# Kernel tuning notes

Hardware: AMD Instinct MI355X
Metric: run time of the kernel (lower is better)

The kernel has to match this reference:

```python
import jax, jax.numpy as jnp
import numpy as np

N = 512      # num_nodes
B = 32       # batch
T = 12       # encoder seq_len
HOR = 12     # decoder horizon
U = 64       # rnn_units
K = 2        # max_diffusion_step
M = 2 * K + 1  # num_matrices (2 supports)


def setup_inputs() -> dict:
    key = jax.random.key(0)
    ks = jax.random.split(key, 16)

    # dual random-walk supports: (D^-1 A)^T and (D^-1 A^T)^T, with self loops
    adj = (jax.random.uniform(ks[0], (N, N)) < 32.0 / N).astype(jnp.float32)

    def rw_T(a):
        a = a + jnp.eye(N, dtype=jnp.float32)
        return (a / a.sum(axis=1, keepdims=True)).T

    supports = jnp.stack([rw_T(adj), rw_T(adj.T)])  # (2, N, N)

    def w(k, shape, s=0.1):
        return jax.random.normal(k, shape, dtype=jnp.float32) * s

    Cin0 = (1 + U) * M   # layer0: input_dim(1)+units, times num_matrices
    Cin1 = (U + U) * M   # layer1
    return {
        "inputs": jax.random.normal(ks[1], (T, B, N * 1), dtype=jnp.float32),
        "supports": supports,
        "enc0_Wg": w(ks[2], (Cin0, 2 * U)), "enc0_bg": jnp.ones(2 * U, jnp.float32),
        "enc0_Wc": w(ks[3], (Cin0, U)),     "enc0_bc": jnp.zeros(U, jnp.float32),
        "enc1_Wg": w(ks[4], (Cin1, 2 * U)), "enc1_bg": jnp.ones(2 * U, jnp.float32),
        "enc1_Wc": w(ks[5], (Cin1, U)),     "enc1_bc": jnp.zeros(U, jnp.float32),
        "dec0_Wg": w(ks[6], (Cin0, 2 * U)), "dec0_bg": jnp.ones(2 * U, jnp.float32),
        "dec0_Wc": w(ks[7], (Cin0, U)),     "dec0_bc": jnp.zeros(U, jnp.float32),
        "dec1_Wg": w(ks[8], (Cin1, 2 * U)), "dec1_bg": jnp.ones(2 * U, jnp.float32),
        "dec1_Wc": w(ks[9], (Cin1, U)),     "dec1_bc": jnp.zeros(U, jnp.float32),
        "proj_W": w(ks[10], (U, 1)),        "proj_b": jnp.zeros(1, jnp.float32),
    }


def reference(inputs, supports, enc0_Wg, enc0_bg, enc0_Wc, enc0_bc,
              enc1_Wg, enc1_bg, enc1_Wc, enc1_bc,
              dec0_Wg, dec0_bg, dec0_Wc, dec0_bc,
              dec1_Wg, dec1_bg, dec1_Wc, dec1_bc, proj_W, proj_b):
    Bsz = inputs.shape[1]

    def gconv(x0, W, b):
        # x0: (B, N, C); Chebyshev-style diffusion over each support
        xs = [x0]
        for i in range(supports.shape[0]):
            s = supports[i]
            x1 = jnp.einsum('ij,bjc->bic', s, x0)
            xs.append(x1)
            xp, xpp = x1, x0
            for _ in range(K - 1):
                x2 = 2.0 * jnp.einsum('ij,bjc->bic', s, xp) - xpp
                xs.append(x2)
                xp, xpp = x2, xp
        # stack on last axis to match torch's (B,N,C,num_matrices) -> (B*N, C*M) layout
        z = jnp.stack(xs, axis=-1).reshape(Bsz, N, -1)
        return z @ W + b

    def cell(x, h, Wg, bg, Wc, bc):
        g = jax.nn.sigmoid(gconv(jnp.concatenate([x, h], axis=-1), Wg, bg))
        r, u = jnp.split(g, 2, axis=-1)
        c = jnp.tanh(gconv(jnp.concatenate([x, r * h], axis=-1), Wc, bc))
        return u * h + (1.0 - u) * c

    h0 = jnp.zeros((Bsz, N, U), inputs.dtype)
    h1 = jnp.zeros((Bsz, N, U), inputs.dtype)

    def enc_step(carry, xt):
        h0, h1 = carry
        x = xt.reshape(Bsz, N, 1)
        h0 = cell(x, h0, enc0_Wg, enc0_bg, enc0_Wc, enc0_bc)
        h1 = cell(h0, h1, enc1_Wg, enc1_bg, enc1_Wc, enc1_bc)
        return (h0, h1), None

    (h0, h1), _ = jax.lax.scan(enc_step, (h0, h1), inputs)

    def dec_step(carry, _):
        h0, h1, xin = carry
        h0 = cell(xin, h0, dec0_Wg, dec0_bg, dec0_Wc, dec0_bc)
        h1 = cell(h0, h1, dec1_Wg, dec1_bg, dec1_Wc, dec1_bc)
        out = h1 @ proj_W + proj_b        # (B, N, 1)
        return (h0, h1, out), out.reshape(Bsz, N)

    go = jnp.zeros((Bsz, N, 1), inputs.dtype)
    _, outs = jax.lax.scan(dec_step, (h0, h1, go), None, length=HOR)
    return outs  # (horizon, B, N*output_dim)
```

## Files before the change

kernel.cpp:

```cpp
#include <hip/hip_runtime.h>
#include <math.h>

#define NN 512
#define BB 32
#define TT 12
#define HH 12
#define UU 64
#define CAP 128
#define RTOT (NN * BB)

__device__ __forceinline__ float sigm(float x) { return 1.f / (1.f + expf(-x)); }

__global__ __launch_bounds__(256) void build_ell(const float* __restrict__ sup,
                                                 int2* __restrict__ ell8,
                                                 int2* __restrict__ ell4,
                                                 int* __restrict__ ecnt) {
    int wave = (blockIdx.x * blockDim.x + threadIdx.x) >> 6;
    int lane = threadIdx.x & 63;
    if (wave >= 2 * NN) return;
    const float* row = sup + (size_t)wave * NN;
    int base = 0;
    for (int k = 0; k < NN / 64; ++k) {
        float v = row[k * 64 + lane];
        unsigned long long m = __ballot(v != 0.0f);
        int pre = __popcll(m & ((1ull << lane) - 1ull));
        if (v != 0.0f) {
            int pos = base + pre;
            if (pos < CAP) {
                int j = k * 64 + lane;
                int vb = __float_as_int(v);
                ell8[(size_t)pos * 1024 + wave] = make_int2(j * 32 + ((j >> 2) & 1) * 16, vb);
                ell4[(size_t)pos * 1024 + wave] = make_int2(j * 16, vb);
            }
        }
        base += __popcll(m);
    }
    if (lane == 0) ecnt[wave] = base < CAP ? base : CAP;
}

__global__ void zero_kernel(float* __restrict__ p, int n) {
    int i = blockIdx.x * 256 + threadIdx.x;
    if (i < n) p[i] = 0.0f;
}

__global__ void wmax_kernel(const int* __restrict__ ecnt, int* __restrict__ wmax) {
    int g = threadIdx.x;
    if (g >= 16) return;
    int s = g >> 3, grp = g & 7;
    int m = 0;
    for (int i = 0; i < 64; ++i) {
        int c = ecnt[s * NN + grp * 64 + i];
        m = c > m ? c : m;
    }
    wmax[g] = m;
}

__global__ void wprep(const float* __restrict__ src, float* __restrict__ dstP,
                      float* __restrict__ dstX, int C, int OO, int WD, int L0) {
    int idx = blockIdx.x * 256 + threadIdx.x;
    int total = 5 * C * OO;
    if (idx >= total) return;
    int oi = idx % WD;
    int rem = idx / WD;
    int c = rem % C;
    int rem2 = rem / C;
    int m = rem2 % 5;
    int oq = rem2 / 5;
    int o = oq * WD + oi;
    int crow = L0 ? (c + 1) : c;
    size_t base = (size_t)crow * 5 * OO + o;
    float v;
    if (m == 0) v = src[base] - src[base + 2 * OO] - src[base + 4 * OO];
    else        v = src[base + (size_t)m * OO];
    dstP[idx] = v;
    if (L0 && c == 0) {
        size_t b0 = (size_t)o;
        float xvv;
        if (m == 0) xvv = src[b0] - src[b0 + 2 * OO] - src[b0 + 4 * OO];
        else        xvv = src[b0 + (size_t)m * OO];
        dstX[(oq * 5 + m) * WD + oi] = xvv;
    }
}

template<bool L0, bool GATE>
__global__ __launch_bounds__(512) void fused(const float* __restrict__ hA,
                                             const float* __restrict__ hB,
                                             const float* __restrict__ g,
                                             const float* __restrict__ Wp,
                                             const float* __restrict__ Xr,
                                             const float* __restrict__ xv,
                                             const float* __restrict__ bias,
                                             const int2* __restrict__ ell,
                                             const int* __restrict__ wmax,
                                             float* __restrict__ gout,
                                             const float* __restrict__ hOld,
                                             float* __restrict__ hNew) {
    constexpr int C  = L0 ? 64 : 128;
    constexpr int WD = GATE ? 8 : 4;

    __shared__ float S[512 * WD * 2];
    float* T0 = S;
    float* T1 = S + 512 * WD;

    int bid = blockIdx.x;
    int swz = (bid & 7) * 64 + (bid >> 3);
    int b = swz >> 4, oq = swz & 15;
    int o0 = oq * WD;
    int n = threadIdx.x;
    int wm0 = wmax[n >> 6];
    int wm1 = wmax[8 + (n >> 6)];
    float xn = L0 ? xv[b * 512 + n] : 0.f;

    const float* Wb = Wp + (size_t)oq * 5 * C * WD;
    float acc[5][WD];
    #pragma unroll
    for (int oi = 0; oi < WD; ++oi) acc[0][oi] = bias[o0 + oi];
    #pragma unroll
    for (int m = 1; m < 5; ++m)
        #pragma unroll
        for (int oi = 0; oi < WD; ++oi) acc[m][oi] = 0.f;

    #pragma unroll 2
    for (int c = 0; c < C; ++c) {
        float a;
        if (L0) {
            if (GATE) a = hA[(size_t)((b << 6) + c) * 512 + n];
            else      a = g[(size_t)((b << 7) + c) * 512 + n];
        } else {
            if (c < 64) {
                a = hA[(size_t)((b << 6) + c) * 512 + n];
            } else {
                int u = c - 64;
                if (GATE) a = hB[(size_t)((b << 6) + u) * 512 + n];
                else      a = g[(size_t)((b << 7) + u) * 512 + n];
            }
        }
        #pragma unroll
        for (int m = 0; m < 5; ++m) {
            const float* wrow = Wb + ((size_t)m * C + c) * WD;
            #pragma unroll
            for (int oi = 0; oi < WD; ++oi)
                acc[m][oi] += a * wrow[oi];
        }
    }

    if (L0) {
        const float* xr = Xr + (size_t)oq * 5 * WD;
        #pragma unroll
        for (int m = 0; m < 5; ++m)
            #pragma unroll
            for (int oi = 0; oi < WD; ++oi)
                acc[m][oi] += xn * xr[m * WD + oi];
    }

    float uval[WD], hval[WD];
    if (!GATE) {
        #pragma unroll
        for (int oi = 0; oi < WD; ++oi) {
            uval[oi] = g[(size_t)((b << 7) + 64 + o0 + oi) * 512 + n];
            hval[oi] = hOld[(size_t)((b << 6) + o0 + oi) * 512 + n];
        }
    }

    int hsel = (n >> 2) & 1;
    if constexpr (WD == 8) {
        *(float4*)&T0[n * 8 + hsel * 4] =
            make_float4(acc[2][0], acc[2][1], acc[2][2], acc[2][3]);
        *(float4*)&T0[n * 8 + (hsel ^ 1) * 4] =
            make_float4(acc[2][4], acc[2][5], acc[2][6], acc[2][7]);
        *(float4*)&T1[n * 8 + hsel * 4] =
            make_float4(acc[4][0], acc[4][1], acc[4][2], acc[4][3]);
        *(float4*)&T1[n * 8 + (hsel ^ 1) * 4] =
            make_float4(acc[4][4], acc[4][5], acc[4][6], acc[4][7]);
    } else {
        *(float4*)&T0[n * 4] = make_float4(acc[2][0], acc[2][1], acc[2][2], acc[2][3]);
        *(float4*)&T1[n * 4] = make_float4(acc[4][0], acc[4][1], acc[4][2], acc[4][3]);
    }

    auto gather = [&](const float* T, const int2* e0, int wm, float* o) {
        const char* Tbyte = (const char*)T;
        float a0[WD];
        #pragma unroll
        for (int i = 0; i < WD; ++i) a0[i] = 0.f;
        #pragma unroll 2
        for (int p = 0; p < wm; ++p) {
            int2 e = e0[(size_t)p << 10];
            float v = __int_as_float(e.y);
            if constexpr (WD == 8) {
                float4 x0 = *(const float4*)(Tbyte + e.x);
                float4 x1 = *(const float4*)(Tbyte + (e.x ^ 16));
                a0[0] += v * x0.x; a0[1] += v * x0.y; a0[2] += v * x0.z; a0[3] += v * x0.w;
                a0[4] += v * x1.x; a0[5] += v * x1.y; a0[6] += v * x1.z; a0[7] += v * x1.w;
            } else {
                float4 x0 = *(const float4*)(Tbyte + e.x);
                a0[0] += v * x0.x; a0[1] += v * x0.y; a0[2] += v * x0.z; a0[3] += v * x0.w;
            }
        }
        #pragma unroll
        for (int i = 0; i < WD; ++i) o[i] = a0[i];
    };
    auto put = [&](float* T, const float* y) {
        if constexpr (WD == 8) {
            *(float4*)&T[n * 8 + hsel * 4]       = make_float4(y[0], y[1], y[2], y[3]);
            *(float4*)&T[n * 8 + (hsel ^ 1) * 4] = make_float4(y[4], y[5], y[6], y[7]);
        } else {
            *(float4*)&T[n * 4] = make_float4(y[0], y[1], y[2], y[3]);
        }
    };

    const int2* e00 = ell + n;
    const int2* e01 = ell + NN + n;
    float g2[WD], g4[WD], t1[WD];

    __syncthreads();

    gather(T0, e00, wm0, t1);
    #pragma unroll
    for (int oi = 0; oi < WD; ++oi) acc[1][oi] += 2.f * t1[oi];
    gather(T1, e01, wm1, t1);
    #pragma unroll
    for (int oi = 0; oi < WD; ++oi) acc[3][oi] += 2.f * t1[oi];

    __syncthreads();

    put(T0, acc[1]);
    put(T1, acc[3]);

    __syncthreads();

    gather(T0, e00, wm0, g2);
    gather(T1, e01, wm1, g4);

    #pragma unroll
    for (int oi = 0; oi < WD; ++oi) {
        float accf = acc[0][oi] + g2[oi] + g4[oi];
        if (GATE) {
            float s = sigm(accf);
            if (oq < 8) {
                const float* hG = L0 ? hA : hB;
                float hv = hG[(size_t)((b << 6) + o0 + oi) * 512 + n];
                gout[(size_t)((b << 7) + o0 + oi) * 512 + n] = s * hv;
            } else {
                gout[(size_t)((b << 7) + o0 + oi) * 512 + n] = s;
            }
        } else {
            float cv = tanhf(accf);
            hNew[(size_t)((b << 6) + o0 + oi) * 512 + n] =
                uval[oi] * hval[oi] + (1.f - uval[oi]) * cv;
        }
    }
}

__global__ void proj_kernel(const float* __restrict__ h1, const float* __restrict__ pW,
                            const float* __restrict__ pb, float* __restrict__ outt) {
    int r = blockIdx.x * 256 + threadIdx.x;
    if (r >= RTOT) return;
    int b = r >> 9, n = r & 511;
    float acc = pb[0];
    #pragma unroll 16
    for (int u = 0; u < 64; ++u)
        acc += h1[(size_t)((b << 6) + u) * 512 + n] * pW[u];
    outt[b * NN + n] = acc;
}

extern "C" void kernel_launch(void* const* d_in, const int* in_sizes, int n_in,
                              void* d_out, int out_size, void* d_ws, size_t ws_size,
                              hipStream_t stream) {
    const float* inputs   = (const float*)d_in[0];
    const float* supports = (const float*)d_in[1];
    const float* enc0_Wg = (const float*)d_in[2];
    const float* enc0_bg = (const float*)d_in[3];
    const float* enc0_Wc = (const float*)d_in[4];
    const float* enc0_bc = (const float*)d_in[5];
    const float* enc1_Wg = (const float*)d_in[6];
    const float* enc1_bg = (const float*)d_in[7];
    const float* enc1_Wc = (const float*)d_in[8];
    const float* enc1_bc = (const float*)d_in[9];
    const float* dec0_Wg = (const float*)d_in[10];
    const float* dec0_bg = (const float*)d_in[11];
    const float* dec0_Wc = (const float*)d_in[12];
    const float* dec0_bc = (const float*)d_in[13];
    const float* dec1_Wg = (const float*)d_in[14];
    const float* dec1_bg = (const float*)d_in[15];
    const float* dec1_Wc = (const float*)d_in[16];
    const float* dec1_bc = (const float*)d_in[17];
    const float* projW   = (const float*)d_in[18];
    const float* projb   = (const float*)d_in[19];
    float* out = (float*)d_out;

    char* wsb = (char*)d_ws;
    size_t off = 0;
    auto alloc = [&](size_t bytes) -> char* {
        char* p = wsb + off;
        off = (off + bytes + 255) & ~(size_t)255;
        return p;
    };
    int2*  ell8  = (int2*)alloc((size_t)CAP * 1024 * 8);
    int2*  ell4  = (int2*)alloc((size_t)CAP * 1024 * 8);
    int*   ecnt  = (int*)alloc((size_t)2 * NN * 4);
    int*   wmax  = (int*)alloc((size_t)16 * 4);
    float* h0a   = (float*)alloc((size_t)RTOT * UU * 4);
    float* h1a   = (float*)alloc((size_t)RTOT * UU * 4);
    float* xzero = (float*)alloc((size_t)RTOT * 4);
    float* h0b   = (float*)alloc((size_t)RTOT * UU * 4);
    float* h1b   = (float*)alloc((size_t)RTOT * UU * 4);
    float* g     = (float*)alloc((size_t)RTOT * 128 * 4);
    float* p_e0g = (float*)alloc((size_t)5 * 64 * 128 * 4);
    float* x_e0g = (float*)alloc((size_t)16 * 5 * 8 * 4);
    float* p_e0c = (float*)alloc((size_t)5 * 64 * 64 * 4);
    float* x_e0c = (float*)alloc((size_t)16 * 5 * 4 * 4);
    float* p_e1g = (float*)alloc((size_t)5 * 128 * 128 * 4);
    float* p_e1c = (float*)alloc((size_t)5 * 128 * 64 * 4);
    float* p_d0g = (float*)alloc((size_t)5 * 64 * 128 * 4);
    float* x_d0g = (float*)alloc((size_t)16 * 5 * 8 * 4);
    float* p_d0c = (float*)alloc((size_t)5 * 64 * 64 * 4);
    float* x_d0c = (float*)alloc((size_t)16 * 5 * 4 * 4);
    float* p_d1g = (float*)alloc((size_t)5 * 128 * 128 * 4);
    float* p_d1c = (float*)alloc((size_t)5 * 128 * 64 * 4);
    float* xdum  = (float*)alloc((size_t)16 * 5 * 8 * 4);
    if (off > ws_size) return;

    {
        int nz = CAP * 1024 * 4;
        zero_kernel<<<(nz + 255) / 256, 256, 0, stream>>>((float*)ell8, nz);
    }
    build_ell<<<256, 256, 0, stream>>>(supports, ell8, ell4, ecnt);
    wmax_kernel<<<1, 16, 0, stream>>>(ecnt, wmax);
    {
        int nz = RTOT * UU * 2 + RTOT;
        zero_kernel<<<(nz + 255) / 256, 256, 0, stream>>>(h0a, nz);
    }
    wprep<<<(5 * 64 * 128 + 255) / 256, 256, 0, stream>>>(enc0_Wg, p_e0g, x_e0g, 64, 128, 8, 1);
    wprep<<<(5 * 64 * 64 + 255) / 256, 256, 0, stream>>>(enc0_Wc, p_e0c, x_e0c, 64, 64, 4, 1);
    wprep<<<(5 * 128 * 128 + 255) / 256, 256, 0, stream>>>(enc1_Wg, p_e1g, xdum, 128, 128, 8, 0);
    wprep<<<(5 * 128 * 64 + 255) / 256, 256, 0, stream>>>(enc1_Wc, p_e1c, xdum, 128, 64, 4, 0);
    wprep<<<(5 * 64 * 128 + 255) / 256, 256, 0, stream>>>(dec0_Wg, p_d0g, x_d0g, 64, 128, 8, 1);
    wprep<<<(5 * 64 * 64 + 255) / 256, 256, 0, stream>>>(dec0_Wc, p_d0c, x_d0c, 64, 64, 4, 1);
    wprep<<<(5 * 128 * 128 + 255) / 256, 256, 0, stream>>>(dec1_Wg, p_d1g, xdum, 128, 128, 8, 0);
    wprep<<<(5 * 128 * 64 + 255) / 256, 256, 0, stream>>>(dec1_Wc, p_d1c, xdum, 128, 64, 4, 0);

    float *h0c = h0a, *h0n = h0b, *h1c = h1a, *h1n = h1b;

    auto cell_l0 = [&](const float* x_bn, const float* Wg_, const float* Xg_,
                       const float* bg_, const float* Wc_, const float* Xc_,
                       const float* bc_) {
        fused<true, true><<<512, 512, 0, stream>>>(h0c, nullptr, g, Wg_, Xg_, x_bn,
                                                   bg_, ell8, wmax, g, nullptr, nullptr);
        fused<true, false><<<512, 512, 0, stream>>>(h0c, nullptr, g, Wc_, Xc_, x_bn,
                                                    bc_, ell4, wmax, nullptr, h0c, h0n);
        float* t = h0c; h0c = h0n; h0n = t;
    };
    auto cell_l1 = [&](const float* Wg_, const float* bg_,
                       const float* Wc_, const float* bc_) {
        fused<false, true><<<512, 512, 0, stream>>>(h0c, h1c, g, Wg_, nullptr, nullptr,
                                                    bg_, ell8, wmax, g, nullptr, nullptr);
        fused<false, false><<<512, 512, 0, stream>>>(h0c, h1c, g, Wc_, nullptr, nullptr,
                                                     bc_, ell4, wmax, nullptr, h1c, h1n);
        float* t = h1c; h1c = h1n; h1n = t;
    };

    for (int t = 0; t < TT; ++t) {
        cell_l0(inputs + (size_t)t * BB * NN, p_e0g, x_e0g, enc0_bg, p_e0c, x_e0c, enc0_bc);
        cell_l1(p_e1g, enc1_bg, p_e1c, enc1_bc);
    }
    for (int t = 0; t < HH; ++t) {
        const float* xin = (t == 0) ? xzero : (out + (size_t)(t - 1) * BB * NN);
        cell_l0(xin, p_d0g, x_d0g, dec0_bg, p_d0c, x_d0c, dec0_bc);
        cell_l1(p_d1g, dec1_bg, p_d1c, dec1_bc);
        proj_kernel<<<(RTOT + 255) / 256, 256, 0, stream>>>(h1c, projW, projb,
                                                            out + (size_t)t * BB * NN);
    }
}
```

Before: 4.771 ms.

## Reorder ELL entries by bank class with per-row rotation to reduce conflicts

Rewrites the ELL construction so each thread handles one support row and places nonzeros interleaved by a bank/quadrant class (derived from the column index), rotated by row. Neighbouring rows are meant to access different banks or channels at the same ELL position during the diffusion SpMM, which cuts conflicts in the gather. The build kernel becomes a serial per-row scan with 16 blocks of 64 threads, so it is much slower than the ballot version, but it runs only once per call.

```diff
diff --git a/kernel.cpp b/kernel.cpp
--- a/kernel.cpp
+++ b/kernel.cpp
@@ -11,31 +11,62 @@
 
 __device__ __forceinline__ float sigm(float x) { return 1.f / (1.f + expf(-x)); }
 
-__global__ __launch_bounds__(256) void build_ell(const float* __restrict__ sup,
-                                                 int2* __restrict__ ell8,
-                                                 int2* __restrict__ ell4,
-                                                 int* __restrict__ ecnt) {
-    int wave = (blockIdx.x * blockDim.x + threadIdx.x) >> 6;
-    int lane = threadIdx.x & 63;
-    if (wave >= 2 * NN) return;
-    const float* row = sup + (size_t)wave * NN;
-    int base = 0;
-    for (int k = 0; k < NN / 64; ++k) {
-        float v = row[k * 64 + lane];
-        unsigned long long m = __ballot(v != 0.0f);
-        int pre = __popcll(m & ((1ull << lane) - 1ull));
+__global__ __launch_bounds__(64) void build_ell(const float* __restrict__ sup,
+                                                int2* __restrict__ ell8,
+                                                int2* __restrict__ ell4,
+                                                int* __restrict__ ecnt) {
+    int r = blockIdx.x * 64 + threadIdx.x;
+    if (r >= 2 * NN) return;
+    const float* row = sup + (size_t)r * NN;
+    int rot = r & 7;
+
+    int c8[8], c4[8], k8[8], k4[8];
+    for (int q = 0; q < 8; ++q) { c8[q] = 0; c4[q] = 0; k8[q] = 0; k4[q] = 0; }
+
+    for (int j = 0; j < NN; ++j) {
+        if (row[j] != 0.0f) {
+            int q8 = (2 * j + ((j >> 2) & 1)) & 7;
+            c8[q8]++;
+            c4[j & 7]++;
+        }
+    }
+
+    int total = 0;
+    for (int j = 0; j < NN; ++j) {
+        float v = row[j];
         if (v != 0.0f) {
-            int pos = base + pre;
-            if (pos < CAP) {
-                int j = k * 64 + lane;
-                int vb = __float_as_int(v);
-                ell8[(size_t)pos * 1024 + wave] = make_int2(j * 32 + ((j >> 2) & 1) * 16, vb);
-                ell4[(size_t)pos * 1024 + wave] = make_int2(j * 16, vb);
+            int vb = __float_as_int(v);
+            {
+                int q = (2 * j + ((j >> 2) & 1)) & 7;
+                int d = (q - rot) & 7;
+                int k = k8[q]++;
+                int pos = 0;
+                for (int dd = 0; dd < 8; ++dd) {
+                    int cq = c8[(rot + dd) & 7];
+                    pos += (cq < k ? cq : k);
+                    if (dd < d && cq > k) pos += 1;
+                }
+                if (pos < CAP)
+                    ell8[(size_t)pos * 1024 + r] =
+                        make_int2(j * 32 + ((j >> 2) & 1) * 16, vb);
             }
-        }
-        base += __popcll(m);
-    }
-    if (lane == 0) ecnt[wave] = base < CAP ? base : CAP;
+            {
+                int q = j & 7;
+                int d = (q - rot) & 7;
+                int k = k4[q]++;
+                int pos = 0;
+                for (int dd = 0; dd < 8; ++dd) {
+                    int cq = c4[(rot + dd) & 7];
+                    pos += (cq < k ? cq : k);
+                    if (dd < d && cq > k) pos += 1;
+                }
+                if (pos < CAP)
+                    ell4[(size_t)pos * 1024 + r] = make_int2(j * 16, vb);
+            }
+            ++total;
+        }
+    }
+    ecnt[r] = total < CAP ? total : CAP;
 }
 
 __global__ void zero_kernel(float* __restrict__ p, int n) {
@@ -324,7 +355,7 @@
         int nz = CAP * 1024 * 4;
         zero_kernel<<<(nz + 255) / 256, 256, 0, stream>>>((float*)ell8, nz);
     }
-    build_ell<<<256, 256, 0, stream>>>(supports, ell8, ell4, ecnt);
+    build_ell<<<16, 64, 0, stream>>>(supports, ell8, ell4, ecnt);
     wmax_kernel<<<1, 16, 0, stream>>>(ecnt, wmax);
     {
         int nz = RTOT * UU * 2 + RTOT;
```

Result: slower. 5.023 ms (+5.3%).

## Reorder ELL entries so each slot spreads columns evenly across bank/channel groups

Applied to the files above, without the earlier changes.

Builds the ELL sparse tables in three passes: bucket nonzeros per row by an address-derived group (8 groups), compute a greedy schedule that assigns each row's entries to ELL slot positions so that, at each slot, rows in a 64-row group hit different groups in a balanced way, then scatter into the ELL arrays. The aim is to cut memory bank/channel conflicts when waves gather hidden-state rows during sparse diffusion. It adds a serial single-block scheduling kernel and temporary buffers, and entries beyond 32 per bucket are dropped, which can truncate rows in skewed cases.

```diff
diff --git a/kernel.cpp b/kernel.cpp
--- a/kernel.cpp
+++ b/kernel.cpp
@@ -11,36 +11,137 @@
 
 __device__ __forceinline__ float sigm(float x) { return 1.f / (1.f + expf(-x)); }
 
-__global__ __launch_bounds__(256) void build_ell(const float* __restrict__ sup,
-                                                 int2* __restrict__ ell8,
-                                                 int2* __restrict__ ell4,
+__global__ void zero_kernel(float* __restrict__ p, int n) {
+    int i = blockIdx.x * 256 + threadIdx.x;
+    if (i < n) p[i] = 0.0f;
+}
+
+__global__ __launch_bounds__(256) void ell_pass1(const float* __restrict__ sup,
+                                                 int2* __restrict__ tmp8,
+                                                 int2* __restrict__ tmp4,
+                                                 int* __restrict__ bc8,
+                                                 int* __restrict__ bc4,
                                                  int* __restrict__ ecnt) {
-    int wave = (blockIdx.x * blockDim.x + threadIdx.x) >> 6;
+    int wave = (blockIdx.x * 256 + threadIdx.x) >> 6;
     int lane = threadIdx.x & 63;
     if (wave >= 2 * NN) return;
     const float* row = sup + (size_t)wave * NN;
-    int base = 0;
-    for (int k = 0; k < NN / 64; ++k) {
-        float v = row[k * 64 + lane];
-        unsigned long long m = __ballot(v != 0.0f);
-        int pre = __popcll(m & ((1ull << lane) - 1ull));
-        if (v != 0.0f) {
-            int pos = base + pre;
-            if (pos < CAP) {
-                int j = k * 64 + lane;
-                int vb = __float_as_int(v);
-                ell8[(size_t)pos * 1024 + wave] = make_int2(j * 32 + ((j >> 2) & 1) * 16, vb);
-                ell4[(size_t)pos * 1024 + wave] = make_int2(j * 16, vb);
-            }
-        }
-        base += __popcll(m);
-    }
-    if (lane == 0) ecnt[wave] = base < CAP ? base : CAP;
-}
-
-__global__ void zero_kernel(float* __restrict__ p, int n) {
-    int i = blockIdx.x * 256 + threadIdx.x;
-    if (i < n) p[i] = 0.0f;
+    int base8[8], base4[8];
+    #pragma unroll
+    for (int q = 0; q < 8; ++q) { base8[q] = 0; base4[q] = 0; }
+    int total = 0;
+    for (int k = 0; k < 8; ++k) {
+        int j = k * 64 + lane;
+        float v = row[j];
+        bool nz = (v != 0.0f);
+        int q8 = (2 * j + ((j >> 2) & 1)) & 7;
+        int q4 = j & 7;
+        unsigned long long below = (1ull << lane) - 1ull;
+        #pragma unroll
+        for (int q = 0; q < 8; ++q) {
+            unsigned long long m8 = __ballot(nz && q8 == q);
+            unsigned long long m4 = __ballot(nz && q4 == q);
+            if (nz && q8 == q) {
+                int pos = base8[q] + __popcll(m8 & below);
+                if (pos < 32)
+                    tmp8[((size_t)wave * 8 + q) * 32 + pos] =
+                        make_int2(j * 32 + ((j >> 2) & 1) * 16, __float_as_int(v));
+            }
+            if (nz && q4 == q) {
+                int pos = base4[q] + __popcll(m4 & below);
+                if (pos < 32)
+                    tmp4[((size_t)wave * 8 + q) * 32 + pos] =
+                        make_int2(j * 16, __float_as_int(v));
+            }
+            base8[q] += __popcll(m8);
+            base4[q] += __popcll(m4);
+        }
+        total += __popcll(__ballot(nz));
+    }
+    if (lane == 0) {
+        ecnt[wave] = total < CAP ? total : CAP;
+        #pragma unroll
+        for (int q = 0; q < 8; ++q) {
+            bc8[wave * 8 + q] = base8[q] < 32 ? base8[q] : 32;
+            bc4[wave * 8 + q] = base4[q] < 32 ? base4[q] : 32;
+        }
+    }
+}
+
+__global__ __launch_bounds__(32) void ell_sched(const int* __restrict__ bc8,
+                                                const int* __restrict__ bc4,
+                                                unsigned char* __restrict__ sched8,
+                                                unsigned char* __restrict__ sched4) {
+    __shared__ unsigned char rem[32][64][8];
+    __shared__ unsigned char rowrem[32][64];
+    int t = threadIdx.x;
+    int tbl = t >> 4;
+    int grp = t & 15;
+    const int* bc = tbl ? bc4 : bc8;
+    unsigned char* sched = tbl ? sched4 : sched8;
+    int totrem = 0;
+    for (int r = 0; r < 64; ++r) {
+        int rr = 0;
+        #pragma unroll
+        for (int q = 0; q < 8; ++q) {
+            int c = bc[(grp * 64 + r) * 8 + q];
+            rem[t][r][q] = (unsigned char)c;
+            rr += c;
+        }
+        rowrem[t][r] = (unsigned char)rr;
+        totrem += rr;
+    }
+    for (int p = 0; totrem > 0 && p < CAP; ++p) {
+        int l0 = 0, l1 = 0, l2 = 0, l3 = 0, l4 = 0, l5 = 0, l6 = 0, l7 = 0;
+        for (int r = 0; r < 64; ++r) {
+            if (rowrem[t][r] == 0) continue;
+            int bq = -1, bl = 1 << 20;
+            {
+                int rm, ld;
+                rm = rem[t][r][0]; ld = l0; if (rm > 0 && ld < bl) { bl = ld; bq = 0; }
+                rm = rem[t][r][1]; ld = l1; if (rm > 0 && ld < bl) { bl = ld; bq = 1; }
+                rm = rem[t][r][2]; ld = l2; if (rm > 0 && ld < bl) { bl = ld; bq = 2; }
+                rm = rem[t][r][3]; ld = l3; if (rm > 0 && ld < bl) { bl = ld; bq = 3; }
+                rm = rem[t][r][4]; ld = l4; if (rm > 0 && ld < bl) { bl = ld; bq = 4; }
+                rm = rem[t][r][5]; ld = l5; if (rm > 0 && ld < bl) { bl = ld; bq = 5; }
+                rm = rem[t][r][6]; ld = l6; if (rm > 0 && ld < bl) { bl = ld; bq = 6; }
+                rm = rem[t][r][7]; ld = l7; if (rm > 0 && ld < bl) { bl = ld; bq = 7; }
+            }
+            int k = (int)rem[t][r][bq] - 1;
+            rem[t][r][bq] = (unsigned char)k;
+            rowrem[t][r]--;
+            totrem--;
+            l0 += (bq == 0); l1 += (bq == 1); l2 += (bq == 2); l3 += (bq == 3);
+            l4 += (bq == 4); l5 += (bq == 5); l6 += (bq == 6); l7 += (bq == 7);
+            sched[((size_t)(grp * 64 + r) * 8 + bq) * 32 + k] = (unsigned char)p;
+        }
+    }
+}
+
+__global__ __launch_bounds__(256) void ell_scatter(const int2* __restrict__ tmp8,
+                                                   const int2* __restrict__ tmp4,
+                                                   const int* __restrict__ bc8,
+                                                   const int* __restrict__ bc4,
+                                                   const unsigned char* __restrict__ sched8,
+                                                   const unsigned char* __restrict__ sched4,
+                                                   int2* __restrict__ ell8,
+                                                   int2* __restrict__ ell4) {
+    int wave = (blockIdx.x * 256 + threadIdx.x) >> 6;
+    int lane = threadIdx.x & 63;
+    if (wave >= 2 * NN) return;
+    #pragma unroll
+    for (int i = 0; i < 4; ++i) {
+        int flat = i * 64 + lane;
+        int q = flat >> 5, k = flat & 31;
+        if (k < bc8[wave * 8 + q]) {
+            int p = sched8[((size_t)wave * 8 + q) * 32 + k];
+            ell8[(size_t)p * 1024 + wave] = tmp8[((size_t)wave * 8 + q) * 32 + k];
+        }
+        if (k < bc4[wave * 8 + q]) {
+            int p = sched4[((size_t)wave * 8 + q) * 32 + k];
+            ell4[(size_t)p * 1024 + wave] = tmp4[((size_t)wave * 8 + q) * 32 + k];
+        }
+    }
 }
 
 __global__ void wmax_kernel(const int* __restrict__ ecnt, int* __restrict__ wmax) {
@@ -297,6 +398,12 @@
     };
     int2*  ell8  = (int2*)alloc((size_t)CAP * 1024 * 8);
     int2*  ell4  = (int2*)alloc((size_t)CAP * 1024 * 8);
+    int2*  tmp8  = (int2*)alloc((size_t)1024 * 8 * 32 * 8);
+    int2*  tmp4  = (int2*)alloc((size_t)1024 * 8 * 32 * 8);
+    int*   bc8   = (int*)alloc((size_t)1024 * 8 * 4);
+    int*   bc4   = (int*)alloc((size_t)1024 * 8 * 4);
+    unsigned char* sched8 = (unsigned char*)alloc((size_t)1024 * 8 * 32);
+    unsigned char* sched4 = (unsigned char*)alloc((size_t)1024 * 8 * 32);
     int*   ecnt  = (int*)alloc((size_t)2 * NN * 4);
     int*   wmax  = (int*)alloc((size_t)16 * 4);
     float* h0a   = (float*)alloc((size_t)RTOT * UU * 4);
@@ -324,7 +431,9 @@
         int nz = CAP * 1024 * 4;
         zero_kernel<<<(nz + 255) / 256, 256, 0, stream>>>((float*)ell8, nz);
     }
-    build_ell<<<256, 256, 0, stream>>>(supports, ell8, ell4, ecnt);
+    ell_pass1<<<256, 256, 0, stream>>>(supports, tmp8, tmp4, bc8, bc4, ecnt);
+    ell_sched<<<1, 32, 0, stream>>>(bc8, bc4, sched8, sched4);
+    ell_scatter<<<256, 256, 0, stream>>>(tmp8, tmp4, bc8, bc4, sched8, sched4, ell8, ell4);
     wmax_kernel<<<1, 16, 0, stream>>>(ecnt, wmax);
     {
         int nz = RTOT * UU * 2 + RTOT;
```

New measurement: 5.531 ms. +15.9%, slower.

## Reorder graph nodes by row nonzero count to balance sparse diffusion waves

Applied to the files above, without the earlier changes.

Adds a preprocessing pass that counts nonzeros per support row, sorts nodes by the larger of their two row counts, and rebuilds the ELL tables in permuted node order with column indices remapped. Inputs and outputs are gathered and scattered through the permutation map. Grouping rows of similar length into the same 64-lane wave lowers the per-wave maximum nonzero count (wmax), so fewer padded ELL iterations run in the fused kernels. The cost is a few extra setup launches, a serial single-block prefix sum, and indirect indexing on the input and output of each step.

```diff
diff --git a/kernel.cpp b/kernel.cpp
--- a/kernel.cpp
+++ b/kernel.cpp
@@ -11,14 +11,60 @@
 
 __device__ __forceinline__ float sigm(float x) { return 1.f / (1.f + expf(-x)); }
 
+__global__ void zero_kernel(float* __restrict__ p, int n) {
+    int i = blockIdx.x * 256 + threadIdx.x;
+    if (i < n) p[i] = 0.0f;
+}
+
+__global__ __launch_bounds__(256) void row_counts(const float* __restrict__ sup,
+                                                  int* __restrict__ cnt) {
+    int wave = (blockIdx.x * 256 + threadIdx.x) >> 6;
+    int lane = threadIdx.x & 63;
+    if (wave >= 2 * NN) return;
+    const float* row = sup + (size_t)wave * NN;
+    int c = 0;
+    for (int k = 0; k < 8; ++k)
+        c += __popcll(__ballot(row[k * 64 + lane] != 0.0f));
+    if (lane == 0) cnt[wave] = c;
+}
+
+__global__ __launch_bounds__(512) void perm_build(const int* __restrict__ cnt,
+                                                  int* __restrict__ nmap,
+                                                  int* __restrict__ rankv) {
+    __shared__ int hist[520];
+    __shared__ int keys[512];
+    int n = threadIdx.x;
+    int c0 = cnt[n], c1 = cnt[NN + n];
+    int key = c0 > c1 ? c0 : c1;
+    hist[n] = 0;
+    if (n < 8) hist[512 + n] = 0;
+    __syncthreads();
+    keys[n] = key;
+    atomicAdd(&hist[key], 1);
+    __syncthreads();
+    if (n == 0) {
+        int s = 0;
+        for (int i = 0; i < 520; ++i) { int h = hist[i]; hist[i] = s; s += h; }
+    }
+    __syncthreads();
+    int pos = hist[key];
+    for (int i = 0; i < n; ++i)
+        if (keys[i] == key) ++pos;
+    nmap[pos] = n;
+    rankv[n] = pos;
+}
+
 __global__ __launch_bounds__(256) void build_ell(const float* __restrict__ sup,
+                                                 const int* __restrict__ nmap,
+                                                 const int* __restrict__ rankv,
                                                  int2* __restrict__ ell8,
                                                  int2* __restrict__ ell4,
                                                  int* __restrict__ ecnt) {
     int wave = (blockIdx.x * blockDim.x + threadIdx.x) >> 6;
     int lane = threadIdx.x & 63;
     if (wave >= 2 * NN) return;
-    const float* row = sup + (size_t)wave * NN;
+    int s = wave >> 9, rp = wave & 511;
+    const float* row = sup + ((size_t)s * NN + nmap[rp]) * NN;
     int base = 0;
     for (int k = 0; k < NN / 64; ++k) {
         float v = row[k * 64 + lane];
@@ -27,7 +73,7 @@
         if (v != 0.0f) {
             int pos = base + pre;
             if (pos < CAP) {
-                int j = k * 64 + lane;
+                int j = rankv[k * 64 + lane];
                 int vb = __float_as_int(v);
                 ell8[(size_t)pos * 1024 + wave] = make_int2(j * 32 + ((j >> 2) & 1) * 16, vb);
                 ell4[(size_t)pos * 1024 + wave] = make_int2(j * 16, vb);
@@ -36,11 +82,6 @@
         base += __popcll(m);
     }
     if (lane == 0) ecnt[wave] = base < CAP ? base : CAP;
-}
-
-__global__ void zero_kernel(float* __restrict__ p, int n) {
-    int i = blockIdx.x * 256 + threadIdx.x;
-    if (i < n) p[i] = 0.0f;
 }
 
 __global__ void wmax_kernel(const int* __restrict__ ecnt, int* __restrict__ wmax) {
@@ -89,6 +130,7 @@
                                              const float* __restrict__ Wp,
                                              const float* __restrict__ Xr,
                                              const float* __restrict__ xv,
+                                             const int* __restrict__ nmap,
                                              const float* __restrict__ bias,
                                              const int2* __restrict__ ell,
                                              const int* __restrict__ wmax,
@@ -109,7 +151,7 @@
     int n = threadIdx.x;
     int wm0 = wmax[n >> 6];
     int wm1 = wmax[8 + (n >> 6)];
-    float xn = L0 ? xv[b * 512 + n] : 0.f;
+    float xn = L0 ? xv[b * 512 + nmap[n]] : 0.f;
 
     const float* Wb = Wp + (size_t)oq * 5 * C * WD;
     float acc[5][WD];
@@ -252,7 +294,8 @@
 }
 
 __global__ void proj_kernel(const float* __restrict__ h1, const float* __restrict__ pW,
-                            const float* __restrict__ pb, float* __restrict__ outt) {
+                            const float* __restrict__ pb, const int* __restrict__ nmap,
+                            float* __restrict__ outt) {
     int r = blockIdx.x * 256 + threadIdx.x;
     if (r >= RTOT) return;
     int b = r >> 9, n = r & 511;
@@ -260,7 +303,7 @@
     #pragma unroll 16
     for (int u = 0; u < 64; ++u)
         acc += h1[(size_t)((b << 6) + u) * 512 + n] * pW[u];
-    outt[b * NN + n] = acc;
+    outt[b * NN + nmap[n]] = acc;
 }
 
 extern "C" void kernel_launch(void* const* d_in, const int* in_sizes, int n_in,
@@ -297,6 +340,9 @@
     };
     int2*  ell8  = (int2*)alloc((size_t)CAP * 1024 * 8);
     int2*  ell4  = (int2*)alloc((size_t)CAP * 1024 * 8);
+    int*   cnt   = (int*)alloc((size_t)2 * NN * 4);
+    int*   nmap  = (int*)alloc((size_t)NN * 4);
+    int*   rankv = (int*)alloc((size_t)NN * 4);
     int*   ecnt  = (int*)alloc((size_t)2 * NN * 4);
     int*   wmax  = (int*)alloc((size_t)16 * 4);
     float* h0a   = (float*)alloc((size_t)RTOT * UU * 4);
@@ -324,7 +370,9 @@
         int nz = CAP * 1024 * 4;
         zero_kernel<<<(nz + 255) / 256, 256, 0, stream>>>((float*)ell8, nz);
     }
-    build_ell<<<256, 256, 0, stream>>>(supports, ell8, ell4, ecnt);
+    row_counts<<<256, 256, 0, stream>>>(supports, cnt);
+    perm_build<<<1, 512, 0, stream>>>(cnt, nmap, rankv);
+    build_ell<<<256, 256, 0, stream>>>(supports, nmap, rankv, ell8, ell4, ecnt);
     wmax_kernel<<<1, 16, 0, stream>>>(ecnt, wmax);
     {
         int nz = RTOT * UU * 2 + RTOT;
@@ -344,17 +392,17 @@
     auto cell_l0 = [&](const float* x_bn, const float* Wg_, const float* Xg_,
                        const float* bg_, const float* Wc_, const float* Xc_,
                        const float* bc_) {
-        fused<true, true><<<512, 512, 0, stream>>>(h0c, nullptr, g, Wg_, Xg_, x_bn,
+        fused<true, true><<<512, 512, 0, stream>>>(h0c, nullptr, g, Wg_, Xg_, x_bn, nmap,
                                                    bg_, ell8, wmax, g, nullptr, nullptr);
-        fused<true, false><<<512, 512, 0, stream>>>(h0c, nullptr, g, Wc_, Xc_, x_bn,
+        fused<true, false><<<512, 512, 0, stream>>>(h0c, nullptr, g, Wc_, Xc_, x_bn, nmap,
                                                     bc_, ell4, wmax, nullptr, h0c, h0n);
         float* t = h0c; h0c = h0n; h0n = t;
     };
     auto cell_l1 = [&](const float* Wg_, const float* bg_,
                        const float* Wc_, const float* bc_) {
-        fused<false, true><<<512, 512, 0, stream>>>(h0c, h1c, g, Wg_, nullptr, nullptr,
+        fused<false, true><<<512, 512, 0, stream>>>(h0c, h1c, g, Wg_, nullptr, nullptr, nmap,
                                                     bg_, ell8, wmax, g, nullptr, nullptr);
-        fused<false, false><<<512, 512, 0, stream>>>(h0c, h1c, g, Wc_, nullptr, nullptr,
+        fused<false, false><<<512, 512, 0, stream>>>(h0c, h1c, g, Wc_, nullptr, nullptr, nmap,
                                                      bc_, ell4, wmax, nullptr, h1c, h1n);
         float* t = h1c; h1c = h1n; h1n = t;
     };
@@ -367,7 +415,7 @@
         const float* xin = (t == 0) ? xzero : (out + (size_t)(t - 1) * BB * NN);
         cell_l0(xin, p_d0g, x_d0g, dec0_bg, p_d0c, x_d0c, dec0_bc);
         cell_l1(p_d1g, dec1_bg, p_d1c, dec1_bc);
-        proj_kernel<<<(RTOT + 255) / 256, 256, 0, stream>>>(h1c, projW, projb,
+        proj_kernel<<<(RTOT + 255) / 256, 256, 0, stream>>>(h1c, projW, projb, nmap,
                                                             out + (size_t)t * BB * NN);
     }
 }
```

New measurement: 4.652 ms. 2.5% less time.
